# Optimization experiments

Hardware: AMD Instinct MI355X
Metric: run time of the kernel (lower is better)

The kernel has to match this reference:

```python
import jax, jax.numpy as jnp
import numpy as np

TAU = 1.0  # forward() default temperature

def setup_inputs() -> dict:
    key = jax.random.key(0)
    ks = jax.random.split(key, 6)
    B, T, I, H, O = 1024, 512, 100, 150, 3
    s_ih = 1.0 / np.sqrt(H)  # torch nn.RNN init scale (uniform +-1/sqrt(H)); randn used for simplicity of magnitude
    return {
        "x": jax.random.normal(ks[0], (B, T, I), dtype=jnp.float32),
        "h0": jax.random.normal(ks[1], (B, H), dtype=jnp.float32),  # init=True: h ~ N(0,1)
        "g": jax.random.normal(ks[2], (B, T, O), dtype=jnp.float32),  # gumbel noise (externalized)
        "W_ih": jax.random.normal(ks[3], (H, I), dtype=jnp.float32) * s_ih,
        "W_hh": jax.random.normal(ks[4], (H, H), dtype=jnp.float32) * s_ih,
        "W_fc": jax.random.normal(ks[5], (O, H), dtype=jnp.float32) * s_ih,
    }

def _rnn_relu(x, h0, W_ih, W_hh):
    # x: [B,T,I]; precompute input projection once (batched GEMM), then scan over time.
    xw = jnp.einsum("bti,hi->tbh", x, W_ih)  # [T,B,H]
    def step(h, xw_t):
        h = jax.nn.relu(xw_t + h @ W_hh.T)
        return h, h
    _, hs = jax.lax.scan(step, h0, xw)  # hs: [T,B,H]
    return jnp.transpose(hs, (1, 0, 2))  # [B,T,H]

def reference(x, h0, g, W_ih, W_hh, W_fc):
    hidden = _rnn_relu(x, h0, W_ih, W_hh)           # [B,T,H]
    logits = jnp.einsum("bth,oh->bto", hidden, W_fc)  # [B,T,O]
    # F.gumbel_softmax(hard=True): softmax((logits+g)/tau), straight-through one-hot
    y_soft = jax.nn.softmax((logits + g) / TAU, axis=-1)
    idx = jnp.argmax(y_soft, axis=-1)
    y_hard = jax.nn.one_hot(idx, logits.shape[-1], dtype=y_soft.dtype)
    out = y_soft + jax.lax.stop_gradient(y_hard - y_soft)
    return (out, hidden, logits)
```

## Files before the change

kernel.cpp:

```cpp
#include <hip/hip_runtime.h>

constexpr int NB = 1024;
constexpr int NT = 512;
constexpr int NI = 100;
constexpr int NH = 150;
constexpr int NO = 3;

template<int CTRL>
__device__ __forceinline__ float dpp_add(float v) {
    int t = __builtin_amdgcn_update_dpp(0, __float_as_int(v), CTRL, 0xF, 0xF, true);
    return v + __int_as_float(t);
}

__device__ __forceinline__ void async_copy_f32(const float* src, float* lds_dst) {
    __builtin_amdgcn_global_load_lds(
        (const __attribute__((address_space(1))) void*)src,
        (__attribute__((address_space(3))) void*)lds_dst, 4, 0, 0);
}

constexpr int XR = 64, XTH = 512;
__global__ __launch_bounds__(XTH, 1)
void xw_gemm(const float* __restrict__ x, const float* __restrict__ Wih,
             float* __restrict__ xw)
{
    __shared__ __align__(16) float Wl[152 * NI];
    __shared__ float xT[XR * 101];
    __shared__ float ot[XR * 151];
    const int tid = threadIdx.x;
    const int b0 = blockIdx.x * XR;
    const int t  = blockIdx.y;

    for (int e = tid; e < 152 * 25; e += XTH) {
        int wr = e / 25, k4 = e - wr * 25;
        float4 v = make_float4(0.f, 0.f, 0.f, 0.f);
        if (wr < NH) v = *reinterpret_cast<const float4*>(Wih + (size_t)wr * NI + 4 * k4);
        *reinterpret_cast<float4*>(&Wl[wr * NI + 4 * k4]) = v;
    }
    for (int e = tid; e < XR * 25; e += XTH) {
        int r = e / 25, k4 = e - r * 25;
        float4 v = *reinterpret_cast<const float4*>(x + ((size_t)(b0 + r) * NT + t) * NI + 4 * k4);
        xT[r * 101 + 4 * k4 + 0] = v.x; xT[r * 101 + 4 * k4 + 1] = v.y;
        xT[r * 101 + 4 * k4 + 2] = v.z; xT[r * 101 + 4 * k4 + 3] = v.w;
    }
    __syncthreads();

    const int row = tid & 63;
    const int wv  = tid >> 6;
    float acc[19];
#pragma unroll
    for (int j = 0; j < 19; ++j) acc[j] = 0.f;
    const float* xr = &xT[row * 101];
    const float* wb = &Wl[19 * wv * NI];
    for (int k4 = 0; k4 < 25; ++k4) {
        const float x0 = xr[4 * k4 + 0], x1 = xr[4 * k4 + 1];
        const float x2 = xr[4 * k4 + 2], x3 = xr[4 * k4 + 3];
#pragma unroll
        for (int j = 0; j < 19; ++j) {
            const float4 w4 = *reinterpret_cast<const float4*>(&wb[j * NI + 4 * k4]);
            acc[j] += w4.x * x0; acc[j] += w4.y * x1;
            acc[j] += w4.z * x2; acc[j] += w4.w * x3;
        }
    }
#pragma unroll
    for (int j = 0; j < 19; ++j) {
        const int h = 19 * wv + j;
        if (h < NH) ot[row * 151 + h] = acc[j];
    }
    __syncthreads();

    for (int e = tid; e < XR * 75; e += XTH) {
        int r = e / 75, c2 = e - r * 75;
        float2 v = make_float2(ot[r * 151 + 2 * c2], ot[r * 151 + 2 * c2 + 1]);
        *reinterpret_cast<float2*>(&xw[((size_t)t * NB + b0 + r) * NH + 2 * c2]) = v;
    }
}

constexpr int RTH = 256;
__global__ __launch_bounds__(RTH, 4)
void rnn_rec(const float* __restrict__ xw, const float* __restrict__ h0v,
             const float* __restrict__ g, const float* __restrict__ Whh,
             const float* __restrict__ Wfc, float* __restrict__ out,
             float* __restrict__ hidden, float* __restrict__ logits)
{
    __shared__ __align__(16) float hx[2][160];
    __shared__ __align__(16) float xq[2][152];
    __shared__ float lg[2][4];

    const int tid = threadIdx.x, lane = tid & 63, wv = tid >> 6;
    const int kg = lane & 7, oq = lane >> 3;
    const int oi = wv * 8 + oq;
    const int row = blockIdx.x;

    float Wreg[5][5][4];
#pragma unroll
    for (int j = 0; j < 5; ++j) {
        const int o = oi + 32 * j;
#pragma unroll
        for (int i = 0; i < 5; ++i)
#pragma unroll
            for (int q = 0; q < 4; ++q) {
                const int k = 4 * (kg + 8 * i) + q;
                float v = 0.f;
                if (k < NH) {
                    if (o < NH) v = Whh[o * NH + k];
                    else if (o < NH + NO) v = Wfc[(o - NH) * NH + k];
                }
                Wreg[j][i][q] = v;
            }
    }

    if (tid < NH) hx[0][tid] = h0v[(size_t)row * NH + tid];
    if (tid < 20) { int f = tid / 10, z = tid - 10 * (tid / 10); hx[f][NH + z] = 0.f; }
    {
        const float* s = xw + (size_t)row * NH;
        if (tid < 64) { async_copy_f32(s + tid, &xq[0][0]); async_copy_f32(s + 64 + tid, &xq[0][64]); }
        if (tid < 22) async_copy_f32(s + 128 + tid, &xq[0][128]);
    }
    __syncthreads();

    float* hidb = hidden + (size_t)row * NT * NH;
    const float* gb = g + (size_t)row * NT * NO;
    float* ob = out + (size_t)row * NT * NO;
    float* lb = logits + (size_t)row * NT * NO;

    auto stepf = [&](int t, const float* __restrict__ cur, float* __restrict__ nxt,
                     float* __restrict__ lgc, const float* __restrict__ xv,
                     float* __restrict__ xnxt) {
        if (t + 1 < NT) {
            const float* s = xw + ((size_t)(t + 1) * NB + row) * NH;
            if (tid < 64) { async_copy_f32(s + tid, xnxt); async_copy_f32(s + 64 + tid, xnxt + 64); }
            if (tid < 22) async_copy_f32(s + 128 + tid, xnxt + 128);
        }
        float acc[5];
#pragma unroll
        for (int j = 0; j < 5; ++j) acc[j] = 0.f;
        const float4* c4 = reinterpret_cast<const float4*>(cur);
#pragma unroll
        for (int i = 0; i < 5; ++i) {
            const float4 hv = c4[kg + 8 * i];
#pragma unroll
            for (int j = 0; j < 5; ++j) {
                acc[j] += Wreg[j][i][0] * hv.x; acc[j] += Wreg[j][i][1] * hv.y;
                acc[j] += Wreg[j][i][2] * hv.z; acc[j] += Wreg[j][i][3] * hv.w;
            }
        }
#pragma unroll
        for (int j = 0; j < 5; ++j) {
            float v = acc[j];
            v = dpp_add<0xB1>(v); v = dpp_add<0x4E>(v); v = dpp_add<0x141>(v);
            acc[j] = v;
        }
        if (kg == 0) {
#pragma unroll
            for (int j = 0; j < 5; ++j) {
                const int o = oi + 32 * j;
                if (o < NH) {
                    if (t < NT) {
                        float v = fmaxf(acc[j] + xv[o], 0.f);
                        nxt[o] = v;
                        hidb[(size_t)t * NH + o] = v;
                    }
                } else if (o < NH + NO) lgc[o - NH] = acc[j];
            }
        }
        __syncthreads();
        if (tid == 0 && t >= 1) {
            float l0 = lgc[0], l1 = lgc[1], l2 = lgc[2];
            const float* gp = gb + (size_t)(t - 1) * NO;
            float s0 = l0 + gp[0], s1 = l1 + gp[1], s2 = l2 + gp[2];
            int am = 0; float best = s0;
            if (s1 > best) { best = s1; am = 1; }
            if (s2 > best) am = 2;
            size_t base = (size_t)(t - 1) * NO;
            ob[base + 0] = (am == 0) ? 1.f : 0.f;
            ob[base + 1] = (am == 1) ? 1.f : 0.f;
            ob[base + 2] = (am == 2) ? 1.f : 0.f;
            lb[base + 0] = l0; lb[base + 1] = l1; lb[base + 2] = l2;
        }
    };

    for (int t = 0; t < NT; t += 2) {
        stepf(t,     hx[0], hx[1], lg[0], xq[0], xq[1]);
        stepf(t + 1, hx[1], hx[0], lg[1], xq[1], xq[0]);
    }
    stepf(NT, hx[0], hx[1], lg[0], xq[0], xq[1]);
}

namespace fb {
constexpr int KP = 256, XOFF = 152, ROWS = 2, KG = 16, NCH = 4, NJ = 5, NTH = 512;
__global__ __launch_bounds__(NTH, 2)
void rnn_fused(const float* __restrict__ x, const float* __restrict__ h0,
               const float* __restrict__ g, const float* __restrict__ Wih,
               const float* __restrict__ Whh, const float* __restrict__ Wfc,
               float* __restrict__ out, float* __restrict__ hidden,
               float* __restrict__ logits)
{
    __shared__ __align__(16) float hx[2][ROWS * KP];
    __shared__ float lg[2][ROWS][4];
    const int tid = threadIdx.x, lane = tid & 63, wv = tid >> 6;
    const int kg = lane & 15, oq = lane >> 4, oi = wv * 4 + oq;
    const int row0 = blockIdx.x * ROWS;
    float Wreg[NJ][NCH][4];
#pragma unroll
    for (int j = 0; j < NJ; ++j) {
        const int o = oi + 32 * j;
#pragma unroll
        for (int i = 0; i < NCH; ++i)
#pragma unroll
            for (int q = 0; q < 4; ++q) {
                const int k = 4 * (kg + KG * i) + q;
                float v = 0.f;
                if (o < NH) {
                    if (k < NH) v = Whh[o * NH + k];
                    else if (k >= XOFF && k < XOFF + NI) v = Wih[o * NI + (k - XOFF)];
                } else if (o < NH + NO) {
                    if (k < NH) v = Wfc[(o - NH) * NH + k];
                }
                Wreg[j][i][q] = v;
            }
    }
    for (int e = tid; e < ROWS * NH; e += NTH) {
        int b = e / NH, k = e - b * NH;
        hx[0][b * KP + k] = h0[(row0 + b) * NH + k];
    }
    for (int e = tid; e < ROWS * NI; e += NTH) {
        int b = e / NI, i = e - b * NI;
        hx[0][b * KP + XOFF + i] = x[((size_t)(row0 + b) * NT + 0) * NI + i];
    }
    if (tid < 2 * ROWS * 6) {
        int u = tid; int f = u / (ROWS * 6); u -= f * (ROWS * 6);
        int b = u / 6, z = u - b * 6;
        int k = (z < 2) ? (NH + z) : (252 + z - 2);
        hx[f][b * KP + k] = 0.f;
    }
    __syncthreads();
    const int xb = (tid / 25) & 1, xq = tid - (tid / 25) * 25;
    const float* xrow = x + ((size_t)(row0 + xb) * NT) * NI + 4 * xq;
    float* hidb = hidden + ((size_t)(row0 + (kg & 1)) * NT) * NH;
    const float* grow = g + ((size_t)(row0 + (tid & 1)) * NT) * NO;
    const size_t emitb = ((size_t)(row0 + (tid & 1)) * NT) * NO;
    auto stepf = [&](int t, const float* __restrict__ cur, float* __restrict__ nxt,
                     float (*__restrict__ lgb)[4]) {
        float4 xp = make_float4(0.f, 0.f, 0.f, 0.f);
        const bool do_x = (tid < 50) && (t < NT - 1);
        if (do_x) xp = *reinterpret_cast<const float4*>(xrow + (size_t)(t + 1) * NI);
        float g0 = 0.f, g1 = 0.f, g2 = 0.f;
        const bool do_e = (tid < ROWS) && (t >= 1);
        if (do_e) {
            const float* gp = grow + (size_t)(t - 1) * NO;
            g0 = gp[0]; g1 = gp[1]; g2 = gp[2];
        }
        const float4* cur4 = reinterpret_cast<const float4*>(cur) + kg;
        float acc[NJ][ROWS];
#pragma unroll
        for (int j = 0; j < NJ; ++j)
#pragma unroll
            for (int b = 0; b < ROWS; ++b) acc[j][b] = 0.f;
#pragma unroll
        for (int i = 0; i < NCH; ++i)
#pragma unroll
            for (int b = 0; b < ROWS; ++b) {
                const float4 hv = cur4[b * (KP / 4) + KG * i];
#pragma unroll
                for (int j = 0; j < NJ; ++j) {
                    acc[j][b] += Wreg[j][i][0] * hv.x;
                    acc[j][b] += Wreg[j][i][1] * hv.y;
                    acc[j][b] += Wreg[j][i][2] * hv.z;
                    acc[j][b] += Wreg[j][i][3] * hv.w;
                }
            }
#pragma unroll
        for (int j = 0; j < NJ; ++j)
#pragma unroll
            for (int b = 0; b < ROWS; ++b) {
                float v = acc[j][b];
                v = dpp_add<0xB1>(v); v = dpp_add<0x4E>(v);
                v = dpp_add<0x141>(v); v = dpp_add<0x140>(v);
                acc[j][b] = v;
            }
        if (kg < ROWS) {
            const int b = kg;
#pragma unroll
            for (int j = 0; j < NJ; ++j) {
                const int o = oi + 32 * j;
                if (o < NH) {
                    if (t < NT) {
                        float v = fmaxf(acc[j][b], 0.f);
                        nxt[b * KP + o] = v;
                        hidb[(size_t)t * NH + o] = v;
                    }
                } else if (o < NH + NO) {
                    lgb[b][o - NH] = acc[j][b];
                }
            }
        }
        if (do_x) *reinterpret_cast<float4*>(nxt + xb * KP + XOFF + 4 * xq) = xp;
        __syncthreads();
        if (do_e) {
            float l0 = lgb[tid][0], l1 = lgb[tid][1], l2 = lgb[tid][2];
            float s0 = l0 + g0, s1 = l1 + g1, s2 = l2 + g2;
            int am = 0; float best = s0;
            if (s1 > best) { best = s1; am = 1; }
            if (s2 > best) { am = 2; }
            size_t base = emitb + (size_t)(t - 1) * NO;
            out[base + 0] = (am == 0) ? 1.f : 0.f;
            out[base + 1] = (am == 1) ? 1.f : 0.f;
            out[base + 2] = (am == 2) ? 1.f : 0.f;
            logits[base + 0] = l0;
            logits[base + 1] = l1;
            logits[base + 2] = l2;
        }
    };
    for (int t = 0; t < NT; t += 2) {
        stepf(t,     hx[0], hx[1], lg[0]);
        stepf(t + 1, hx[1], hx[0], lg[1]);
    }
    stepf(NT, hx[0], hx[1], lg[0]);
}
}

extern "C" void kernel_launch(void* const* d_in, const int* in_sizes, int n_in,
                              void* d_out, int out_size, void* d_ws, size_t ws_size,
                              hipStream_t stream) {
    const float* x   = (const float*)d_in[0];
    const float* h0  = (const float*)d_in[1];
    const float* g   = (const float*)d_in[2];
    const float* Wih = (const float*)d_in[3];
    const float* Whh = (const float*)d_in[4];
    const float* Wfc = (const float*)d_in[5];

    float* out    = (float*)d_out;
    float* hidden = out + (size_t)NB * NT * NO;
    float* logits = hidden + (size_t)NB * NT * NH;

    const size_t need = (size_t)NT * NB * NH * sizeof(float);
    if (d_ws != nullptr && ws_size >= need) {
        float* xwbuf = (float*)d_ws;
        hipLaunchKernelGGL(xw_gemm, dim3(NB / XR, NT), dim3(XTH), 0, stream,
                           x, Wih, xwbuf);
        hipLaunchKernelGGL(rnn_rec, dim3(NB), dim3(RTH), 0, stream,
                           xwbuf, h0, g, Whh, Wfc, out, hidden, logits);
    } else {
        hipLaunchKernelGGL(fb::rnn_fused, dim3(NB / fb::ROWS), dim3(fb::NTH), 0, stream,
                           x, h0, g, Wih, Whh, Wfc, out, hidden, logits);
    }
}
```

Measured before the change: 1.558 ms.

## Make xw GEMM persistent with double-buffered x tile prefetch

The input-projection GEMM becomes a persistent kernel of 256 blocks. Each block loads W_ih into LDS once and then loops over 32 (t, batch) tiles. The next tile's x rows are prefetched into registers during the current tile's compute and written into a second LDS buffer, so repeated W_ih loads are amortised and global latency overlaps with FMA work. The output staging pad changes from 151 to 153 and the recurrent kernel's launch bounds drop from 4 to 2 waves per SIMD. The cost is fewer blocks in flight and more registers per thread.

```diff
diff --git a/kernel.cpp b/kernel.cpp
--- a/kernel.cpp
+++ b/kernel.cpp
@@ -18,17 +18,15 @@
         (__attribute__((address_space(3))) void*)lds_dst, 4, 0, 0);
 }
 
-constexpr int XR = 64, XTH = 512;
+constexpr int XR = 64, XTH = 512, NTILES = (NB / XR) * NT, XBLK = 256;
 __global__ __launch_bounds__(XTH, 1)
 void xw_gemm(const float* __restrict__ x, const float* __restrict__ Wih,
              float* __restrict__ xw)
 {
     __shared__ __align__(16) float Wl[152 * NI];
-    __shared__ float xT[XR * 101];
-    __shared__ float ot[XR * 151];
+    __shared__ float xT[2][XR * 101];
+    __shared__ float ot[XR * 153];
     const int tid = threadIdx.x;
-    const int b0 = blockIdx.x * XR;
-    const int t  = blockIdx.y;
 
     for (int e = tid; e < 152 * 25; e += XTH) {
         int wr = e / 25, k4 = e - wr * 25;
@@ -36,47 +34,87 @@
         if (wr < NH) v = *reinterpret_cast<const float4*>(Wih + (size_t)wr * NI + 4 * k4);
         *reinterpret_cast<float4*>(&Wl[wr * NI + 4 * k4]) = v;
     }
-    for (int e = tid; e < XR * 25; e += XTH) {
-        int r = e / 25, k4 = e - r * 25;
-        float4 v = *reinterpret_cast<const float4*>(x + ((size_t)(b0 + r) * NT + t) * NI + 4 * k4);
-        xT[r * 101 + 4 * k4 + 0] = v.x; xT[r * 101 + 4 * k4 + 1] = v.y;
-        xT[r * 101 + 4 * k4 + 2] = v.z; xT[r * 101 + 4 * k4 + 3] = v.w;
+
+    const int row = tid & 63;
+    const int hg  = tid >> 6;
+    const int tile0 = blockIdx.x * (NTILES / XBLK);
+
+    auto tile_t = [](int id) { return id >> 4; };
+    auto tile_b = [](int id) { return (id & 15) * XR; };
+
+    {
+        const int t = tile_t(tile0), b0 = tile_b(tile0);
+        for (int e = tid; e < XR * 25; e += XTH) {
+            int r = e / 25, k4 = e - r * 25;
+            float4 v = *reinterpret_cast<const float4*>(
+                x + ((size_t)(b0 + r) * NT + t) * NI + 4 * k4);
+            float* d = &xT[0][r * 101 + 4 * k4];
+            d[0] = v.x; d[1] = v.y; d[2] = v.z; d[3] = v.w;
+        }
     }
     __syncthreads();
 
-    const int row = tid & 63;
-    const int wv  = tid >> 6;
-    float acc[19];
-#pragma unroll
-    for (int j = 0; j < 19; ++j) acc[j] = 0.f;
-    const float* xr = &xT[row * 101];
-    const float* wb = &Wl[19 * wv * NI];
-    for (int k4 = 0; k4 < 25; ++k4) {
-        const float x0 = xr[4 * k4 + 0], x1 = xr[4 * k4 + 1];
-        const float x2 = xr[4 * k4 + 2], x3 = xr[4 * k4 + 3];
+    int cur = 0;
+    for (int it = 0; it < NTILES / XBLK; ++it) {
+        const int id = tile0 + it;
+        const int t = tile_t(id), b0 = tile_b(id);
+
+        float4 pre[4];
+        int preN = 0;
+        if (it + 1 < NTILES / XBLK) {
+            const int t2 = tile_t(id + 1), b2 = tile_b(id + 1);
+            for (int e = tid; e < XR * 25; e += XTH) {
+                int r = e / 25, k4 = e - r * 25;
+                pre[preN++] = *reinterpret_cast<const float4*>(
+                    x + ((size_t)(b2 + r) * NT + t2) * NI + 4 * k4);
+            }
+        }
+
+        float acc[19];
+#pragma unroll
+        for (int j = 0; j < 19; ++j) acc[j] = 0.f;
+        const float* xr = &xT[cur][row * 101];
+        const float* wb = &Wl[19 * hg * NI];
+        for (int k4 = 0; k4 < 25; ++k4) {
+            const float x0 = xr[4 * k4 + 0], x1 = xr[4 * k4 + 1];
+            const float x2 = xr[4 * k4 + 2], x3 = xr[4 * k4 + 3];
+#pragma unroll
+            for (int j = 0; j < 19; ++j) {
+                const float4 w4 = *reinterpret_cast<const float4*>(&wb[j * NI + 4 * k4]);
+                acc[j] += w4.x * x0; acc[j] += w4.y * x1;
+                acc[j] += w4.z * x2; acc[j] += w4.w * x3;
+            }
+        }
+
+        __syncthreads();
+
 #pragma unroll
         for (int j = 0; j < 19; ++j) {
-            const float4 w4 = *reinterpret_cast<const float4*>(&wb[j * NI + 4 * k4]);
-            acc[j] += w4.x * x0; acc[j] += w4.y * x1;
-            acc[j] += w4.z * x2; acc[j] += w4.w * x3;
-        }
-    }
-#pragma unroll
-    for (int j = 0; j < 19; ++j) {
-        const int h = 19 * wv + j;
-        if (h < NH) ot[row * 151 + h] = acc[j];
-    }
-    __syncthreads();
-
-    for (int e = tid; e < XR * 75; e += XTH) {
-        int r = e / 75, c2 = e - r * 75;
-        float2 v = make_float2(ot[r * 151 + 2 * c2], ot[r * 151 + 2 * c2 + 1]);
-        *reinterpret_cast<float2*>(&xw[((size_t)t * NB + b0 + r) * NH + 2 * c2]) = v;
+            const int h = 19 * hg + j;
+            if (h < NH) ot[row * 153 + h] = acc[j];
+        }
+        if (it + 1 < NTILES / XBLK) {
+            int n = 0;
+            for (int e = tid; e < XR * 25; e += XTH) {
+                int r = e / 25, k4 = e - r * 25;
+                float* d = &xT[cur ^ 1][r * 101 + 4 * k4];
+                float4 v = pre[n++];
+                d[0] = v.x; d[1] = v.y; d[2] = v.z; d[3] = v.w;
+            }
+        }
+        __syncthreads();
+
+        for (int e = tid; e < XR * 75; e += XTH) {
+            int r = e / 75, c2 = e - r * 75;
+            float2 v = make_float2(ot[r * 153 + 2 * c2], ot[r * 153 + 2 * c2 + 1]);
+            *reinterpret_cast<float2*>(&xw[((size_t)t * NB + b0 + r) * NH + 2 * c2]) = v;
+        }
+        cur ^= 1;
     }
 }
 
 constexpr int RTH = 256;
-__global__ __launch_bounds__(RTH, 4)
+__global__ __launch_bounds__(RTH, 2)
 void rnn_rec(const float* __restrict__ xw, const float* __restrict__ h0v,
              const float* __restrict__ g, const float* __restrict__ Whh,
              const float* __restrict__ Wfc, float* __restrict__ out,
@@ -336,7 +374,7 @@
     const size_t need = (size_t)NT * NB * NH * sizeof(float);
     if (d_ws != nullptr && ws_size >= need) {
         float* xwbuf = (float*)d_ws;
-        hipLaunchKernelGGL(xw_gemm, dim3(NB / XR, NT), dim3(XTH), 0, stream,
+        hipLaunchKernelGGL(xw_gemm, dim3(XBLK), dim3(XTH), 0, stream,
                            x, Wih, xwbuf);
         hipLaunchKernelGGL(rnn_rec, dim3(NB), dim3(RTH), 0, stream,
                            xwbuf, h0, g, Whh, Wfc, out, hidden, logits);
```

Measured after the change: 2.066 ms. 1.33x slower.

## Restructure input-projection GEMM: lanes own output columns, x rows streamed from global

Applied to the files above, without the earlier changes.

The xw_gemm kernel is rewritten so each block stages W_ih in LDS once and loops over 16 timesteps. Each lane owns three hidden columns, and each wave processes 8 batch rows. The x rows are loaded straight from global memory as uniform float4 broadcasts with double-buffered prefetch, which removes the per-timestep x transpose and the output staging through LDS. This amortizes the weight load across timesteps and allows two blocks per CU, at the cost of more register pressure and scalar-like broadcast global loads.

```diff
diff --git a/kernel.cpp b/kernel.cpp
--- a/kernel.cpp
+++ b/kernel.cpp
@@ -18,60 +18,101 @@
         (__attribute__((address_space(3))) void*)lds_dst, 4, 0, 0);
 }
 
-constexpr int XR = 64, XTH = 512;
-__global__ __launch_bounds__(XTH, 1)
+constexpr int XTH = 512;
+constexpr int XROWS = 64;
+constexpr int XTPB = 16;
+constexpr int XBLKS = (NB / XROWS) * (NT / XTPB);
+__global__ __launch_bounds__(XTH, 2)
 void xw_gemm(const float* __restrict__ x, const float* __restrict__ Wih,
              float* __restrict__ xw)
 {
-    __shared__ __align__(16) float Wl[152 * NI];
-    __shared__ float xT[XR * 101];
-    __shared__ float ot[XR * 151];
-    const int tid = threadIdx.x;
-    const int b0 = blockIdx.x * XR;
-    const int t  = blockIdx.y;
-
-    for (int e = tid; e < 152 * 25; e += XTH) {
-        int wr = e / 25, k4 = e - wr * 25;
+    __shared__ float Wl[192 * 101];
+    const int tid  = threadIdx.x;
+    const int lane = tid & 63;
+    const int wvu  = __builtin_amdgcn_readfirstlane(tid >> 6);
+    const int b0 = (blockIdx.x & 15) * XROWS;
+    const int t0 = (blockIdx.x >> 4) * XTPB;
+
+    for (int e = tid; e < 192 * 25; e += XTH) {
+        int r = e / 25, k4 = e - r * 25;
         float4 v = make_float4(0.f, 0.f, 0.f, 0.f);
-        if (wr < NH) v = *reinterpret_cast<const float4*>(Wih + (size_t)wr * NI + 4 * k4);
-        *reinterpret_cast<float4*>(&Wl[wr * NI + 4 * k4]) = v;
-    }
-    for (int e = tid; e < XR * 25; e += XTH) {
-        int r = e / 25, k4 = e - r * 25;
-        float4 v = *reinterpret_cast<const float4*>(x + ((size_t)(b0 + r) * NT + t) * NI + 4 * k4);
-        xT[r * 101 + 4 * k4 + 0] = v.x; xT[r * 101 + 4 * k4 + 1] = v.y;
-        xT[r * 101 + 4 * k4 + 2] = v.z; xT[r * 101 + 4 * k4 + 3] = v.w;
+        if (r < NH) v = *reinterpret_cast<const float4*>(Wih + (size_t)r * NI + 4 * k4);
+        float* d = &Wl[r * 101 + 4 * k4];
+        d[0] = v.x; d[1] = v.y; d[2] = v.z; d[3] = v.w;
     }
     __syncthreads();
 
-    const int row = tid & 63;
-    const int wv  = tid >> 6;
-    float acc[19];
-#pragma unroll
-    for (int j = 0; j < 19; ++j) acc[j] = 0.f;
-    const float* xr = &xT[row * 101];
-    const float* wb = &Wl[19 * wv * NI];
-    for (int k4 = 0; k4 < 25; ++k4) {
-        const float x0 = xr[4 * k4 + 0], x1 = xr[4 * k4 + 1];
-        const float x2 = xr[4 * k4 + 2], x3 = xr[4 * k4 + 3];
-#pragma unroll
-        for (int j = 0; j < 19; ++j) {
-            const float4 w4 = *reinterpret_cast<const float4*>(&wb[j * NI + 4 * k4]);
-            acc[j] += w4.x * x0; acc[j] += w4.y * x1;
-            acc[j] += w4.z * x2; acc[j] += w4.w * x3;
-        }
-    }
-#pragma unroll
-    for (int j = 0; j < 19; ++j) {
-        const int h = 19 * wv + j;
-        if (h < NH) ot[row * 151 + h] = acc[j];
-    }
-    __syncthreads();
-
-    for (int e = tid; e < XR * 75; e += XTH) {
-        int r = e / 75, c2 = e - r * 75;
-        float2 v = make_float2(ot[r * 151 + 2 * c2], ot[r * 151 + 2 * c2 + 1]);
-        *reinterpret_cast<float2*>(&xw[((size_t)t * NB + b0 + r) * NH + 2 * c2]) = v;
+    const float* wl0 = &Wl[lane * 101];
+    const float* wl1 = &Wl[(lane + 64) * 101];
+    const float* wl2 = &Wl[(lane + 128) * 101];
+    const int rowbase = b0 + 8 * wvu;
+
+    for (int tt = 0; tt < XTPB; ++tt) {
+        const int t = t0 + tt;
+        const float* xr[8];
+#pragma unroll
+        for (int r = 0; r < 8; ++r)
+            xr[r] = x + ((size_t)(rowbase + r) * NT + t) * NI;
+
+        float acc[8][3];
+#pragma unroll
+        for (int r = 0; r < 8; ++r) { acc[r][0] = 0.f; acc[r][1] = 0.f; acc[r][2] = 0.f; }
+
+        auto fma_step = [&](const float4& w0, const float4& w1, const float4& w2,
+                            const float4 (&xb)[8]) {
+#pragma unroll
+            for (int r = 0; r < 8; ++r) {
+                const float4 xv = xb[r];
+                acc[r][0] += w0.x * xv.x; acc[r][0] += w0.y * xv.y;
+                acc[r][0] += w0.z * xv.z; acc[r][0] += w0.w * xv.w;
+                acc[r][1] += w1.x * xv.x; acc[r][1] += w1.y * xv.y;
+                acc[r][1] += w1.z * xv.z; acc[r][1] += w1.w * xv.w;
+                acc[r][2] += w2.x * xv.x; acc[r][2] += w2.y * xv.y;
+                acc[r][2] += w2.z * xv.z; acc[r][2] += w2.w * xv.w;
+            }
+        };
+        auto ldx = [&](int r, int k4) {
+            return *reinterpret_cast<const float4*>(xr[r] + 4 * k4);
+        };
+
+        float4 bufA[8], bufB[8];
+#pragma unroll
+        for (int r = 0; r < 8; ++r) bufA[r] = ldx(r, 0);
+
+#pragma unroll
+        for (int k2 = 0; k2 < 12; ++k2) {
+            const int k4 = 2 * k2;
+#pragma unroll
+            for (int r = 0; r < 8; ++r) bufB[r] = ldx(r, k4 + 1);
+            {
+                float4 w0 = *reinterpret_cast<const float4*>(wl0 + 4 * k4);
+                float4 w1 = *reinterpret_cast<const float4*>(wl1 + 4 * k4);
+                float4 w2 = *reinterpret_cast<const float4*>(wl2 + 4 * k4);
+                fma_step(w0, w1, w2, bufA);
+            }
+#pragma unroll
+            for (int r = 0; r < 8; ++r) bufA[r] = ldx(r, k4 + 2);
+            {
+                float4 w0 = *reinterpret_cast<const float4*>(wl0 + 4 * (k4 + 1));
+                float4 w1 = *reinterpret_cast<const float4*>(wl1 + 4 * (k4 + 1));
+                float4 w2 = *reinterpret_cast<const float4*>(wl2 + 4 * (k4 + 1));
+                fma_step(w0, w1, w2, bufB);
+            }
+        }
+        {
+            float4 w0 = *reinterpret_cast<const float4*>(wl0 + 96);
+            float4 w1 = *reinterpret_cast<const float4*>(wl1 + 96);
+            float4 w2 = *reinterpret_cast<const float4*>(wl2 + 96);
+            fma_step(w0, w1, w2, bufA);
+        }
+
+#pragma unroll
+        for (int r = 0; r < 8; ++r) {
+            float* ob = xw + ((size_t)t * NB + rowbase + r) * NH;
+            ob[lane]      = acc[r][0];
+            ob[lane + 64] = acc[r][1];
+            if (lane < NH - 128) ob[lane + 128] = acc[r][2];
+        }
     }
 }
 
@@ -336,7 +377,7 @@
     const size_t need = (size_t)NT * NB * NH * sizeof(float);
     if (d_ws != nullptr && ws_size >= need) {
         float* xwbuf = (float*)d_ws;
-        hipLaunchKernelGGL(xw_gemm, dim3(NB / XR, NT), dim3(XTH), 0, stream,
+        hipLaunchKernelGGL(xw_gemm, dim3(XBLKS), dim3(XTH), 0, stream,
                            x, Wih, xwbuf);
         hipLaunchKernelGGL(rnn_rec, dim3(NB), dim3(RTH), 0, stream,
                            xwbuf, h0, g, Whh, Wfc, out, hidden, logits);
```

Measured after the change: 2.484 ms. 1.59x slower.
